# Optimization experiments

Measured on AMD Instinct MI355X. Metric: run time of the kernel, lower is better.

Reference implementation:

```python
import jax, jax.numpy as jnp
import numpy as np

H = 12  # num_heads


def rotate_half(x):
    x1, x2 = jnp.split(x, 2, axis=-1)
    return jnp.concatenate([-x2, x1], axis=-1)


def setup_inputs() -> dict:
    key = jax.random.key(0)
    ks = jax.random.split(key, 8)
    B, N, C = 4, 2048, 768
    num_special = 5
    Ns = N - num_special
    D = C // H
    x = jax.random.normal(ks[0], (B, N, C), dtype=jnp.float32)
    rope_cos = jax.random.uniform(ks[1], (Ns, D), dtype=jnp.float32)
    rope_sin = jax.random.uniform(ks[2], (Ns, D), dtype=jnp.float32)
    W_qkv = jax.random.normal(ks[3], (C, 3 * C), dtype=jnp.float32) * (C ** -0.5)
    b_qkv = jax.random.normal(ks[4], (3 * C,), dtype=jnp.float32) * 0.02
    W_proj = jax.random.normal(ks[5], (C, C), dtype=jnp.float32) * (C ** -0.5)
    b_proj = jax.random.normal(ks[6], (C,), dtype=jnp.float32) * 0.02
    return {"x": x, "rope_cos": rope_cos, "rope_sin": rope_sin,
            "W_qkv": W_qkv, "b_qkv": b_qkv, "W_proj": W_proj, "b_proj": b_proj,
            "num_special": num_special}


def reference(x, rope_cos, rope_sin, W_qkv, b_qkv, W_proj, b_proj, num_special):
    B, N, C = x.shape
    D = C // H
    scale = D ** -0.5
    qkv = (x @ W_qkv + b_qkv).reshape(B, N, 3, H, D)
    qkv = jnp.transpose(qkv, (2, 0, 3, 1, 4))  # [3, B, H, N, D]
    q, k, v = qkv[0], qkv[1], qkv[2]
    # partial RoPE: special tokens untouched, spatial tokens rotated
    q_spec, q_spat = q[:, :, :num_special], q[:, :, num_special:]
    k_spec, k_spat = k[:, :, :num_special], k[:, :, num_special:]
    q_spat = q_spat * rope_cos + rotate_half(q_spat) * rope_sin
    k_spat = k_spat * rope_cos + rotate_half(k_spat) * rope_sin
    q = jnp.concatenate([q_spec, q_spat], axis=2)
    k = jnp.concatenate([k_spec, k_spat], axis=2)
    attn = jnp.einsum('bhqd,bhkd->bhqk', q, k) * scale  # [B,H,N,N]
    attn = jax.nn.softmax(attn, axis=-1)
    out = jnp.einsum('bhqk,bhkd->bhqd', attn, v)  # [B,H,N,D]
    out = jnp.transpose(out, (0, 2, 1, 3)).reshape(B, N, C)
    return out @ W_proj + b_proj
```

## Files before the change

### kernel.cpp

```cpp
#include <hip/hip_runtime.h>
#include <stdint.h>

typedef unsigned short u16;
typedef __bf16 bf16x8 __attribute__((ext_vector_type(8)));
typedef short s16x4 __attribute__((ext_vector_type(4)));
typedef float f32x4 __attribute__((ext_vector_type(4)));

typedef __attribute__((address_space(1))) void gvoid_t;
typedef __attribute__((address_space(3))) void lvoid_t;

struct alignas(16) U128 { uint32_t x, y, z, w; };
struct alignas(16) F128 { float x, y, z, w; };
struct alignas(8)  U64v { uint32_t x, y; };

__device__ __forceinline__ void gld16(const u16* g, u16* lds) {
  __builtin_amdgcn_global_load_lds((gvoid_t*)const_cast<u16*>(g),
                                   (lvoid_t*)lds, 16, 0, 0);
}

__device__ __forceinline__ u16 f2bf(float f) {
  uint32_t u = __builtin_bit_cast(uint32_t, f);
  u += 0x7FFFu + ((u >> 16) & 1u);
  return (u16)(u >> 16);
}
__device__ __forceinline__ float bf2f(u16 h) {
  return __builtin_bit_cast(float, (uint32_t)h << 16);
}
__device__ __forceinline__ bf16x8 ldfrag(const u16* p) {
  U128 u = *reinterpret_cast<const U128*>(p);
  return __builtin_bit_cast(bf16x8, u);
}
__device__ __forceinline__ uint32_t pkbf(float a, float b) {
  uint32_t ua = __builtin_bit_cast(uint32_t, a) + 0x8000u;
  uint32_t ub = __builtin_bit_cast(uint32_t, b) + 0x8000u;
  return (ua >> 16) | (ub & 0xFFFF0000u);
}

__device__ __forceinline__ float EXP2(float x) { return __builtin_amdgcn_exp2f(x); }

__global__ void cvt_f32_bf16(const float* __restrict__ in, u16* __restrict__ out) {
  int i = (blockIdx.x * 256 + threadIdx.x) * 4;
  F128 v = *reinterpret_cast<const F128*>(in + i);
  U64v o;
  o.x = (uint32_t)f2bf(v.x) | ((uint32_t)f2bf(v.y) << 16);
  o.y = (uint32_t)f2bf(v.z) | ((uint32_t)f2bf(v.w) << 16);
  *reinterpret_cast<U64v*>(out + i) = o;
}

__global__ void transpose_cvt(const float* __restrict__ W, u16* __restrict__ Wt,
                              int K, int N) {
  __shared__ float T[32][33];
  const int n0 = blockIdx.x * 32, k0 = blockIdx.y * 32;
  const int tid = threadIdx.x;
#pragma unroll
  for (int i = 0; i < 4; ++i) {
    int e = i * 256 + tid, r = e >> 5, c = e & 31;
    T[r][c] = W[(size_t)(k0 + r) * N + n0 + c];
  }
  __syncthreads();
#pragma unroll
  for (int i = 0; i < 4; ++i) {
    int e = i * 256 + tid, r = e >> 5, c = e & 31;
    Wt[(size_t)(n0 + r) * K + k0 + c] = f2bf(T[c][r]);
  }
}

__global__ __launch_bounds__(256, 2)
void gemm_bt(const u16* __restrict__ A, const u16* __restrict__ Bt,
             const float* __restrict__ bias, float* __restrict__ C,
             int M, int N, int K) {
  __shared__ u16 As[2][128 * 32];
  __shared__ u16 Bs[2][128 * 32];
  const int tid = threadIdx.x;
  const int wave = tid >> 6, lane = tid & 63;
  const int quad = lane >> 4, l16 = lane & 15;
  const int m0 = blockIdx.y * 128, n0 = blockIdx.x * 128;
  const int wr = (wave & 1) * 64, wc = (wave >> 1) * 64;

  f32x4 acc[4][4];
#pragma unroll
  for (int i = 0; i < 4; ++i)
#pragma unroll
    for (int j = 0; j < 4; ++j) acc[i][j] = (f32x4){0.f, 0.f, 0.f, 0.f};

  const int c0 = wave * 2 * 64 + lane;
  const int row0 = c0 >> 2, kq0 = c0 & 3;
  const int c1 = c0 + 64;
  const int row1 = c1 >> 2, kq1 = c1 & 3;

#define STAGE_G(k0_, s_)                                                       \
  do {                                                                         \
    gld16(A + (size_t)(m0 + row0) * K + (k0_) + kq0 * 8, &As[s_][wave * 1024]);\
    gld16(Bt + (size_t)(n0 + row0) * K + (k0_) + kq0 * 8, &Bs[s_][wave * 1024]);\
    gld16(A + (size_t)(m0 + row1) * K + (k0_) + kq1 * 8, &As[s_][wave * 1024 + 512]); \
    gld16(Bt + (size_t)(n0 + row1) * K + (k0_) + kq1 * 8, &Bs[s_][wave * 1024 + 512]); \
  } while (0)

  STAGE_G(0, 0);
  __syncthreads();

  int cur = 0;
  for (int k0 = 0; k0 < K; k0 += 32, cur ^= 1) {
    if (k0 + 32 < K) STAGE_G(k0 + 32, cur ^ 1);
    bf16x8 af[4], bfr[4];
#pragma unroll
    for (int rb = 0; rb < 4; ++rb) af[rb] = ldfrag(&As[cur][(wr + rb * 16 + l16) * 32 + quad * 8]);
#pragma unroll
    for (int cb = 0; cb < 4; ++cb) bfr[cb] = ldfrag(&Bs[cur][(wc + cb * 16 + l16) * 32 + quad * 8]);
#pragma unroll
    for (int rb = 0; rb < 4; ++rb)
#pragma unroll
      for (int cb = 0; cb < 4; ++cb)
        acc[rb][cb] = __builtin_amdgcn_mfma_f32_16x16x32_bf16(af[rb], bfr[cb], acc[rb][cb], 0, 0, 0);
    __syncthreads();
  }
#pragma unroll
  for (int cb = 0; cb < 4; ++cb) {
    int col = n0 + wc + cb * 16 + l16;
    float bv = bias[col];
#pragma unroll
    for (int rb = 0; rb < 4; ++rb) {
#pragma unroll
      for (int r = 0; r < 4; ++r) {
        int row = m0 + wr + rb * 16 + quad * 4 + r;
        C[(size_t)row * N + col] = acc[rb][cb][r] + bv;
      }
    }
  }
#undef STAGE_G
}

__global__ __launch_bounds__(256, 2)
void gemm_qkv_rope(const u16* __restrict__ A, const u16* __restrict__ Bt,
                   const float* __restrict__ bias,
                   const float* __restrict__ cosT, const float* __restrict__ sinT,
                   const int* __restrict__ nsp,
                   u16* __restrict__ Qo, u16* __restrict__ Ko, u16* __restrict__ Vto) {
  __shared__ u16 As[2][128 * 32];
  __shared__ u16 Bs[2][128 * 32];
  const int K = 768;
  const int tid = threadIdx.x;
  const int wave = tid >> 6, lane = tid & 63;
  const int quad = lane >> 4, l16 = lane & 15;
  const int m0 = blockIdx.y * 128, n0 = blockIdx.x * 128;
  const int wr = (wave & 1) * 64, wc = (wave >> 1) * 64;

  f32x4 acc[4][4];
#pragma unroll
  for (int i = 0; i < 4; ++i)
#pragma unroll
    for (int j = 0; j < 4; ++j) acc[i][j] = (f32x4){0.f, 0.f, 0.f, 0.f};

  const int c0 = wave * 2 * 64 + lane;
  const int row0 = c0 >> 2, kq0 = c0 & 3;
  const int c1 = c0 + 64;
  const int row1 = c1 >> 2, kq1 = c1 & 3;

#define STAGE_G(k0_, s_)                                                       \
  do {                                                                         \
    gld16(A + (size_t)(m0 + row0) * K + (k0_) + kq0 * 8, &As[s_][wave * 1024]);\
    gld16(Bt + (size_t)(n0 + row0) * K + (k0_) + kq0 * 8, &Bs[s_][wave * 1024]);\
    gld16(A + (size_t)(m0 + row1) * K + (k0_) + kq1 * 8, &As[s_][wave * 1024 + 512]); \
    gld16(Bt + (size_t)(n0 + row1) * K + (k0_) + kq1 * 8, &Bs[s_][wave * 1024 + 512]); \
  } while (0)

  STAGE_G(0, 0);
  __syncthreads();

  int cur = 0;
  for (int k0 = 0; k0 < K; k0 += 32, cur ^= 1) {
    if (k0 + 32 < K) STAGE_G(k0 + 32, cur ^ 1);
    bf16x8 af[4], bfr[4];
#pragma unroll
    for (int rb = 0; rb < 4; ++rb) af[rb] = ldfrag(&As[cur][(wr + rb * 16 + l16) * 32 + quad * 8]);
#pragma unroll
    for (int cb = 0; cb < 4; ++cb) bfr[cb] = ldfrag(&Bs[cur][(wc + cb * 16 + l16) * 32 + quad * 8]);
#pragma unroll
    for (int rb = 0; rb < 4; ++rb)
#pragma unroll
      for (int cb = 0; cb < 4; ++cb)
        acc[rb][cb] = __builtin_amdgcn_mfma_f32_16x16x32_bf16(af[rb], bfr[cb], acc[rb][cb], 0, 0, 0);
    __syncthreads();
  }
#undef STAGE_G

  const int sec = blockIdx.x / 6;
  const int gcol0 = n0 + wc;
  const int hh = (gcol0 >> 6) % 12;
  const int bb = m0 >> 11;
  const int nbase = m0 & 2047;
  const int bh = bb * 12 + hh;
  const int num_special = nsp[0];
  const float QS = 0.125f * 1.4426950408889634f;

  if (sec < 2) {
    u16* outp = sec ? Ko : Qo;
    const float qs = sec ? 1.0f : QS;
#pragma unroll
    for (int cbp = 0; cbp < 2; ++cbp) {
      const int d1 = cbp * 16 + l16;
      const int d2 = d1 + 32;
      const float bv1 = bias[gcol0 + d1];
      const float bv2 = bias[gcol0 + d2];
#pragma unroll
      for (int rb = 0; rb < 4; ++rb) {
#pragma unroll
        for (int r = 0; r < 4; ++r) {
          const int n = nbase + wr + rb * 16 + quad * 4 + r;
          float v1 = acc[rb][cbp][r] + bv1;
          float v2 = acc[rb][cbp + 2][r] + bv2;
          float o1, o2;
          if (n < num_special) {
            o1 = v1; o2 = v2;
          } else {
            int ns = n - num_special;
            float c1 = cosT[ns * 64 + d1], s1 = sinT[ns * 64 + d1];
            float c2 = cosT[ns * 64 + d2], s2 = sinT[ns * 64 + d2];
            o1 = v1 * c1 - v2 * s1;
            o2 = v2 * c2 + v1 * s2;
          }
          size_t ob = ((size_t)bh * 2048 + n) * 64;
          outp[ob + d1] = f2bf(o1 * qs);
          outp[ob + d2] = f2bf(o2 * qs);
        }
      }
    }
  } else {
#pragma unroll
    for (int cb = 0; cb < 4; ++cb) {
      const int d = cb * 16 + l16;
      const float bv = bias[gcol0 + d];
#pragma unroll
      for (int rb = 0; rb < 4; ++rb) {
        const int nr = nbase + wr + rb * 16 + quad * 4;
        U64v o;
        o.x = (uint32_t)f2bf(acc[rb][cb][0] + bv) |
              ((uint32_t)f2bf(acc[rb][cb][1] + bv) << 16);
        o.y = (uint32_t)f2bf(acc[rb][cb][2] + bv) |
              ((uint32_t)f2bf(acc[rb][cb][3] + bv) << 16);
        *(U64v*)&Vto[((size_t)bh * 64 + d) * 2048 + nr] = o;
      }
    }
  }
}

__global__ __launch_bounds__(256, 3)
void attn(const u16* __restrict__ Q, const u16* __restrict__ Kg,
          const u16* __restrict__ Vt, u16* __restrict__ Out) {
  __shared__ u16 smem[2 * 8192];
  __shared__ float invS[64];
  const int tid = threadIdx.x;
  const int wave = tid >> 6, lane = tid & 63;
  const int quad = lane >> 4, l16 = lane & 15;
  const int idx = blockIdx.x;
  const int bh = idx % 48, qt = idx / 48;
  const int b = bh / 12, h = bh % 12;
  const u16* Qb = Q + (size_t)bh * 2048 * 64;
  const u16* Kb = Kg + (size_t)bh * 2048 * 64;
  const u16* Vb = Vt + (size_t)bh * 64 * 2048;
  const int wkey0 = wave * 16;

  const int lrow = lane >> 3;
  const int lch  = (lane & 7) ^ (lrow & 7);
  const int r0a = wave * 8;
  const int r0b = 32 + wave * 8;
  const int ksrc_a = (r0a + lrow) * 64 + lch * 8;
  const int ksrc_b = (r0b + lrow) * 64 + lch * 8;
  const size_t vsrc_a = (size_t)(r0a + lrow) * 2048 + lch * 8;
  const size_t vsrc_b = (size_t)(r0b + lrow) * 2048 + lch * 8;

  const int krd = (wkey0 + l16) * 64 + ((quad ^ (l16 & 7)) << 3);
  int vrd[4];
#pragma unroll
  for (int db = 0; db < 4; ++db)
    vrd[db] = (db * 16 + l16) * 64 +
              ((((wave << 1) | (quad >> 1)) ^ (l16 & 7)) << 3) + (quad & 1) * 4;

#define STAGE_A(kt_, s_)                                                      \
  do {                                                                        \
    u16* Kd = smem + (s_) * 8192;                                             \
    u16* Vd = Kd + 4096;                                                      \
    const u16* Ksrc = Kb + (size_t)(kt_) * 4096;                              \
    const u16* Vsrc = Vb + (kt_) * 64;                                        \
    gld16(Ksrc + ksrc_a, Kd + r0a * 64);                                      \
    gld16(Ksrc + ksrc_b, Kd + r0b * 64);                                      \
    gld16(Vsrc + vsrc_a, Vd + r0a * 64);                                      \
    gld16(Vsrc + vsrc_b, Vd + r0b * 64);                                      \
  } while (0)

  bf16x8 qf[4][2];
#pragma unroll
  for (int m = 0; m < 4; ++m) {
    const u16* qp = Qb + (size_t)(qt * 64 + m * 16 + l16) * 64 + quad * 8;
    qf[m][0] = ldfrag(qp);
    qf[m][1] = ldfrag(qp + 32);
  }

  f32x4 oacc[4][4];
#pragma unroll
  for (int m = 0; m < 4; ++m)
#pragma unroll
    for (int db = 0; db < 4; ++db) oacc[m][db] = (f32x4){0.f, 0.f, 0.f, 0.f};
  float psum[4] = {0.f, 0.f, 0.f, 0.f};

  STAGE_A(0, 0);
  __syncthreads();

  for (int kt = 0; kt < 32; ++kt) {
    const int cur = kt & 1;
    if (kt < 31) STAGE_A(kt + 1, cur ^ 1);
    const u16* Ksh = smem + cur * 8192;
    const u16* Vsh = Ksh + 4096;

    bf16x8 ka0 = ldfrag(Ksh + krd);
    bf16x8 ka1 = ldfrag(Ksh + (krd ^ 32));

    s16x4 pf[4];
#pragma unroll
    for (int m = 0; m < 4; ++m) {
      f32x4 st = (f32x4){0.f, 0.f, 0.f, 0.f};
      st = __builtin_amdgcn_mfma_f32_16x16x32_bf16(ka0, qf[m][0], st, 0, 0, 0);
      st = __builtin_amdgcn_mfma_f32_16x16x32_bf16(ka1, qf[m][1], st, 0, 0, 0);
      float p0 = EXP2(st[0]);
      float p1 = EXP2(st[1]);
      float p2 = EXP2(st[2]);
      float p3 = EXP2(st[3]);
      psum[m] += (p0 + p1) + (p2 + p3);
      U64v pd;
      pd.x = pkbf(p0, p1);
      pd.y = pkbf(p2, p3);
      pf[m] = __builtin_bit_cast(s16x4, pd);
    }

#pragma unroll
    for (int db = 0; db < 4; ++db) {
      s16x4 vf = __builtin_bit_cast(s16x4, *(const U64v*)(Vsh + vrd[db]));
#pragma unroll
      for (int m = 0; m < 4; ++m)
        oacc[m][db] = __builtin_amdgcn_mfma_f32_16x16x16bf16_1k(pf[m], vf, oacc[m][db], 0, 0, 0);
    }
    __syncthreads();
  }
#undef STAGE_A

#pragma unroll
  for (int m = 0; m < 4; ++m) {
    psum[m] += __shfl_xor(psum[m], 16, 64);
    psum[m] += __shfl_xor(psum[m], 32, 64);
  }
  float* LS = (float*)smem;
  if (quad == 0) {
#pragma unroll
    for (int m = 0; m < 4; ++m) LS[wave * 64 + m * 16 + l16] = psum[m];
  }
  __syncthreads();
  if (tid < 64) {
    float tot = LS[tid] + LS[64 + tid] + LS[128 + tid] + LS[192 + tid];
    invS[tid] = 1.0f / tot;
  }

  float* OR = (float*)smem;
  const int q = tid >> 2;
  const int d0 = (tid & 3) * 4;
  const size_t obase = ((size_t)(b * 2048 + qt * 64 + q)) * 768 + h * 64 + d0;
#pragma unroll
  for (int db = 0; db < 4; ++db) {
    __syncthreads();
#pragma unroll
    for (int m = 0; m < 4; ++m)
#pragma unroll
      for (int r = 0; r < 4; ++r)
        OR[(wave * 64 + m * 16 + quad * 4 + r) * 18 + l16] = oacc[m][db][r];
    __syncthreads();
    float s0 = 0.f, s1 = 0.f, s2 = 0.f, s3 = 0.f;
#pragma unroll
    for (int w = 0; w < 4; ++w) {
      const float* p = &OR[(w * 64 + q) * 18 + d0];
      s0 += p[0]; s1 += p[1]; s2 += p[2]; s3 += p[3];
    }
    float iv = invS[q];
    U64v o;
    o.x = (uint32_t)f2bf(s0 * iv) | ((uint32_t)f2bf(s1 * iv) << 16);
    o.y = (uint32_t)f2bf(s2 * iv) | ((uint32_t)f2bf(s3 * iv) << 16);
    *(U64v*)&Out[obase + db * 16] = o;
  }
}

extern "C" void kernel_launch(void* const* d_in, const int* in_sizes, int n_in,
                              void* d_out, int out_size, void* d_ws, size_t ws_size,
                              hipStream_t stream) {
  (void)in_sizes; (void)n_in; (void)out_size; (void)ws_size;
  const float* x        = (const float*)d_in[0];
  const float* rope_cos = (const float*)d_in[1];
  const float* rope_sin = (const float*)d_in[2];
  const float* W_qkv    = (const float*)d_in[3];
  const float* b_qkv    = (const float*)d_in[4];
  const float* W_proj   = (const float*)d_in[5];
  const float* b_proj   = (const float*)d_in[6];
  const int*   nsp      = (const int*)d_in[7];
  float* out = (float*)d_out;

  char* ws = (char*)d_ws;
  u16* Xb   = (u16*)(ws);
  u16* Wqkt = (u16*)(ws + 12582912);
  u16* Wpt  = (u16*)(ws + 16121856);
  u16* Qb   = (u16*)(ws + 55050240);
  u16* Kb   = (u16*)(ws + 67633152);
  u16* Vtb  = (u16*)(ws + 80216064);
  u16* att  = (u16*)(ws + 92798976);

  cvt_f32_bf16<<<6144, 256, 0, stream>>>(x, Xb);
  transpose_cvt<<<dim3(72, 24), 256, 0, stream>>>(W_qkv, Wqkt, 768, 2304);
  transpose_cvt<<<dim3(24, 24), 256, 0, stream>>>(W_proj, Wpt, 768, 768);
  gemm_qkv_rope<<<dim3(18, 64), 256, 0, stream>>>(Xb, Wqkt, b_qkv, rope_cos, rope_sin,
                                                  nsp, Qb, Kb, Vtb);
  attn<<<1536, 256, 0, stream>>>(Qb, Kb, Vtb, att);
  gemm_bt<<<dim3(6, 64), 256, 0, stream>>>(att, Wpt, b_proj, out, 8192, 768, 768);
}
```

Before: 247.3 us.

## Software-pipeline attention loop so PV MFMAs overlap next tile's QK and exp

```diff
diff --git a/kernel.cpp b/kernel.cpp
--- a/kernel.cpp
+++ b/kernel.cpp
@@ -3,6 +3,7 @@
 
 typedef unsigned short u16;
 typedef __bf16 bf16x8 __attribute__((ext_vector_type(8)));
+typedef __bf16 bf16x2 __attribute__((ext_vector_type(2)));
 typedef short s16x4 __attribute__((ext_vector_type(4)));
 typedef float f32x4 __attribute__((ext_vector_type(4)));
 
@@ -31,9 +32,10 @@
   return __builtin_bit_cast(bf16x8, u);
 }
 __device__ __forceinline__ uint32_t pkbf(float a, float b) {
-  uint32_t ua = __builtin_bit_cast(uint32_t, a) + 0x8000u;
-  uint32_t ub = __builtin_bit_cast(uint32_t, b) + 0x8000u;
-  return (ua >> 16) | (ub & 0xFFFF0000u);
+  bf16x2 v;
+  v[0] = (__bf16)a;
+  v[1] = (__bf16)b;
+  return __builtin_bit_cast(uint32_t, v);
 }
 
 __device__ __forceinline__ float EXP2(float x) { return __builtin_amdgcn_exp2f(x); }
@@ -304,43 +306,69 @@
   float psum[4] = {0.f, 0.f, 0.f, 0.f};
 
   STAGE_A(0, 0);
-  __syncthreads();
-
-  for (int kt = 0; kt < 32; ++kt) {
-    const int cur = kt & 1;
-    if (kt < 31) STAGE_A(kt + 1, cur ^ 1);
-    const u16* Ksh = smem + cur * 8192;
-    const u16* Vsh = Ksh + 4096;
-
+  STAGE_A(1, 1);
+  __syncthreads();
+
+  s16x4 pf[4];
+  U64v  vfc[4];
+  {
+    const u16* Ksh = smem;
+    const u16* Vsh = smem + 4096;
     bf16x8 ka0 = ldfrag(Ksh + krd);
     bf16x8 ka1 = ldfrag(Ksh + (krd ^ 32));
-
-    s16x4 pf[4];
+#pragma unroll
+    for (int db = 0; db < 4; ++db) vfc[db] = *(const U64v*)(Vsh + vrd[db]);
 #pragma unroll
     for (int m = 0; m < 4; ++m) {
       f32x4 st = (f32x4){0.f, 0.f, 0.f, 0.f};
       st = __builtin_amdgcn_mfma_f32_16x16x32_bf16(ka0, qf[m][0], st, 0, 0, 0);
       st = __builtin_amdgcn_mfma_f32_16x16x32_bf16(ka1, qf[m][1], st, 0, 0, 0);
-      float p0 = EXP2(st[0]);
-      float p1 = EXP2(st[1]);
-      float p2 = EXP2(st[2]);
-      float p3 = EXP2(st[3]);
+      float p0 = EXP2(st[0]), p1 = EXP2(st[1]), p2 = EXP2(st[2]), p3 = EXP2(st[3]);
       psum[m] += (p0 + p1) + (p2 + p3);
-      U64v pd;
-      pd.x = pkbf(p0, p1);
-      pd.y = pkbf(p2, p3);
+      U64v pd; pd.x = pkbf(p0, p1); pd.y = pkbf(p2, p3);
       pf[m] = __builtin_bit_cast(s16x4, pd);
     }
-
-#pragma unroll
-    for (int db = 0; db < 4; ++db) {
-      s16x4 vf = __builtin_bit_cast(s16x4, *(const U64v*)(Vsh + vrd[db]));
-#pragma unroll
-      for (int m = 0; m < 4; ++m)
-        oacc[m][db] = __builtin_amdgcn_mfma_f32_16x16x16bf16_1k(pf[m], vf, oacc[m][db], 0, 0, 0);
+  }
+  __syncthreads();
+
+  for (int kt = 0; kt < 31; ++kt) {
+    const int cur = kt & 1, nxt = cur ^ 1;
+    const u16* Kshn = smem + nxt * 8192;
+    const u16* Vshn = Kshn + 4096;
+    bf16x8 kn0 = ldfrag(Kshn + krd);
+    bf16x8 kn1 = ldfrag(Kshn + (krd ^ 32));
+    U64v vfn[4];
+#pragma unroll
+    for (int db = 0; db < 4; ++db) vfn[db] = *(const U64v*)(Vshn + vrd[db]);
+
+    if (kt < 30) STAGE_A(kt + 2, cur);
+
+    s16x4 pfn[4];
+#pragma unroll
+    for (int m = 0; m < 4; ++m) {
+      f32x4 st = (f32x4){0.f, 0.f, 0.f, 0.f};
+      st = __builtin_amdgcn_mfma_f32_16x16x32_bf16(kn0, qf[m][0], st, 0, 0, 0);
+      st = __builtin_amdgcn_mfma_f32_16x16x32_bf16(kn1, qf[m][1], st, 0, 0, 0);
+#pragma unroll
+      for (int db = 0; db < 4; ++db)
+        oacc[m][db] = __builtin_amdgcn_mfma_f32_16x16x16bf16_1k(pf[m], __builtin_bit_cast(s16x4, vfc[db]), oacc[m][db], 0, 0, 0);
+      float p0 = EXP2(st[0]), p1 = EXP2(st[1]), p2 = EXP2(st[2]), p3 = EXP2(st[3]);
+      psum[m] += (p0 + p1) + (p2 + p3);
+      U64v pd; pd.x = pkbf(p0, p1); pd.y = pkbf(p2, p3);
+      pfn[m] = __builtin_bit_cast(s16x4, pd);
     }
     __syncthreads();
-  }
+#pragma unroll
+    for (int m = 0; m < 4; ++m) pf[m] = pfn[m];
+#pragma unroll
+    for (int db = 0; db < 4; ++db) vfc[db] = vfn[db];
+  }
+
+#pragma unroll
+  for (int m = 0; m < 4; ++m)
+#pragma unroll
+    for (int db = 0; db < 4; ++db)
+      oacc[m][db] = __builtin_amdgcn_mfma_f32_16x16x16bf16_1k(pf[m], __builtin_bit_cast(s16x4, vfc[db]), oacc[m][db], 0, 0, 0);
 #undef STAGE_A
 
 #pragma unroll
@@ -348,6 +376,7 @@
     psum[m] += __shfl_xor(psum[m], 16, 64);
     psum[m] += __shfl_xor(psum[m], 32, 64);
   }
+  __syncthreads();
   float* LS = (float*)smem;
   if (quad == 0) {
 #pragma unroll
```

After: 255.4 us. 3.3% more time.
